# Kernel tuning notes

Hardware: AMD Instinct MI355X
Metric: run time of the kernel (lower is better)

Reference implementation:

```python
import jax, jax.numpy as jnp
import numpy as np

HIDDEN = 1024
NH = 4
DK = 1024          # key_dim = hidden * expand_k
DV = 2048          # value_dim = hidden * expand_v
HDK = DK // NH     # 256
HDV = DV // NH     # 512
LOWRANK = 16
GATE_NORM = 16.0
CHUNK = 64
EPS = 1e-5


def setup_inputs() -> dict:
    key = jax.random.key(0)
    ks = jax.random.split(key, 10)
    s = 0.02  # xavier-ish init scale (gain 2**-2.5)
    return {
        "hidden_states": jax.random.normal(ks[0], (4, 2048, HIDDEN), dtype=jnp.float32),
        "Wq": jax.random.normal(ks[1], (HIDDEN, DK), dtype=jnp.float32) * s,
        "Wk": jax.random.normal(ks[2], (HIDDEN, DK), dtype=jnp.float32) * s,
        "Wv": jax.random.normal(ks[3], (HIDDEN, DV), dtype=jnp.float32) * s,
        "Wg": jax.random.normal(ks[4], (HIDDEN, DV), dtype=jnp.float32) * s,
        "Wgk1": jax.random.normal(ks[5], (HIDDEN, LOWRANK), dtype=jnp.float32) * s,
        "Wgk2": jax.random.normal(ks[6], (LOWRANK, DK), dtype=jnp.float32) * s,
        "bgk2": jnp.zeros((DK,), dtype=jnp.float32),
        "g_norm_w": jnp.ones((HDV,), dtype=jnp.float32),
        "Wo": jax.random.normal(ks[7], (DV, HIDDEN), dtype=jnp.float32) * s,
    }


def _gla_chunked(q, k, v, gk):
    """Chunked gated linear attention.
    q, k, gk: [B, H, L, dk]; v: [B, H, L, dv]. Recurrence:
      S_t = diag(exp(gk_t)) S_{t-1} + k_t^T v_t ; o_t = (q_t * scale) S_t
    """
    B, H, L, dk = q.shape
    dv = v.shape[-1]
    N = L // CHUNK
    scale = dk ** -0.5

    def split(x):  # [B,H,L,d] -> [N,B,H,C,d]
        x = x.reshape(B, H, N, CHUNK, x.shape[-1])
        return jnp.moveaxis(x, 2, 0)

    qc, kc, vc, gc = split(q), split(k), split(v), split(gk)
    mask = jnp.tril(jnp.ones((CHUNK, CHUNK), dtype=bool))

    def step(S, inp):
        q_c, k_c, v_c, g_c = inp                 # [B,H,C,dk] / [B,H,C,dv]
        b = jnp.cumsum(g_c, axis=2)              # inclusive cumulative log-decay
        b_last = b[:, :, -1:, :]                 # [B,H,1,dk]
        q_g = q_c * jnp.exp(b) * scale           # decayed queries
        k_intra = k_c * jnp.exp(-b)              # for intra-chunk scores
        k_state = k_c * jnp.exp(b_last - b)      # for state update
        # intra-chunk causal scores: s_ij = q_i k_j exp(b_i - b_j), j <= i
        scores = jnp.einsum('bhid,bhjd->bhij', q_g, k_intra)
        scores = jnp.where(mask, scores, 0.0)
        o_intra = jnp.einsum('bhij,bhjv->bhiv', scores, v_c)
        o_inter = jnp.einsum('bhid,bhdv->bhiv', q_g, S)
        S_new = S * jnp.exp(b_last[:, :, 0, :])[..., None] \
            + jnp.einsum('bhcd,bhcv->bhdv', k_state, v_c)
        return S_new, o_intra + o_inter

    S0 = jnp.zeros((B, H, dk, dv), dtype=q.dtype)
    _, o = jax.lax.scan(step, S0, (qc, kc, vc, gc))
    o = jnp.moveaxis(o, 0, 2).reshape(B, H, L, dv)
    return o


def reference(hidden_states, Wq, Wk, Wv, Wg, Wgk1, Wgk2, bgk2, g_norm_w, Wo):
    B, L, _ = hidden_states.shape
    h = hidden_states

    def heads(x, hd):  # [B,L,H*hd] -> [B,H,L,hd]
        return x.reshape(B, L, NH, hd).transpose(0, 2, 1, 3)

    q = heads(h @ Wq, HDK)
    k = heads(h @ Wk, HDK)
    v = heads(h @ Wv, HDV)
    gk_raw = (h @ Wgk1) @ Wgk2 + bgk2
    gk = jax.nn.log_sigmoid(gk_raw) / GATE_NORM
    gk = heads(gk, HDK)

    o = _gla_chunked(q, k, v, gk)                # [B,H,L,hdv]
    o = o.transpose(0, 2, 1, 3)                  # [B,L,H,hdv]

    # FusedRMSNormSwishGate: rmsnorm(o) * silu(g), per head_v_dim
    g = (h @ Wg).reshape(B, L, NH, HDV)
    rms = o * jax.lax.rsqrt(jnp.mean(o * o, axis=-1, keepdims=True) + EPS)
    o = rms * g_norm_w * (g * jax.nn.sigmoid(g))
    o = o.reshape(B, L, DV)
    return o @ Wo
```

## Files before the change

kernel.cpp:

```cpp
#include <hip/hip_runtime.h>
#include <stdint.h>


typedef float f32x4 __attribute__((ext_vector_type(4)));
typedef short s16x8 __attribute__((ext_vector_type(8)));
typedef short s16x4 __attribute__((ext_vector_type(4)));

#define DEVINL __device__ __forceinline__

DEVINL short f2bf(float f) {
  union { float f; uint32_t u; } v; v.f = f;
  uint32_t r = v.u + 0x7fffu + ((v.u >> 16) & 1u);
  return (short)(r >> 16);
}
DEVINL float bf2f(short s) {
  union { uint32_t u; float f; } v; v.u = ((uint32_t)(uint16_t)s) << 16;
  return v.f;
}
DEVINL f32x4 mfma16(s16x8 a, s16x8 b, f32x4 c) {
  return __builtin_amdgcn_mfma_f32_16x16x32_bf16(a, b, c, 0, 0, 0);
}
#define ASYNC_COPY16(G, L)                                                   \
  __builtin_amdgcn_global_load_lds(                                          \
      (__attribute__((address_space(1))) void*)(void*)(G),                   \
      (__attribute__((address_space(3))) void*)(L), 16, 0, 0)

__global__ __launch_bounds__(256) void cvt_f2b_vec(const float* __restrict__ src,
                                                   short* __restrict__ dst) {
  int id = blockIdx.x * 256 + threadIdx.x;
  f32x4 v = ((const f32x4*)src)[id];
  s16x4 o = { f2bf(v[0]), f2bf(v[1]), f2bf(v[2]), f2bf(v[3]) };
  ((s16x4*)dst)[id] = o;
}

__global__ __launch_bounds__(256) void transpose_weights(
    const float* __restrict__ Wq, const float* __restrict__ Wk,
    const float* __restrict__ Wv, const float* __restrict__ Wg,
    const float* __restrict__ Wo, short* __restrict__ wT,
    short* __restrict__ woT) {
  __shared__ short sh[64 * 66];
  const float* src; short* dst; int K, N;
  switch (blockIdx.z) {
    case 0: src = Wq; dst = wT;                         K = 1024; N = 1024; break;
    case 1: src = Wk; dst = wT + (size_t)1024 * 1024;   K = 1024; N = 1024; break;
    case 2: src = Wv; dst = wT + (size_t)2048 * 1024;   K = 1024; N = 2048; break;
    case 3: src = Wg; dst = wT + (size_t)4096 * 1024;   K = 1024; N = 2048; break;
    default: src = Wo; dst = woT;                       K = 2048; N = 1024; break;
  }
  int n0 = blockIdx.x * 64, k0 = blockIdx.y * 64;
  if (n0 >= N || k0 >= K) return;
  int tx = threadIdx.x & 63, ty = threadIdx.x >> 6;
#pragma unroll
  for (int j = 0; j < 16; j++) {
    int r = j * 4 + ty;
    sh[r * 66 + tx] = f2bf(src[(size_t)(k0 + r) * N + n0 + tx]);
  }
  __syncthreads();
#pragma unroll
  for (int j = 0; j < 16; j++) {
    int r = j * 4 + ty;
    dst[(size_t)(n0 + r) * K + k0 + tx] = sh[tx * 66 + r];
  }
}

__global__ __launch_bounds__(256) void transpose_s16_batched(const short* __restrict__ src,
                                                             short* __restrict__ dst,
                                                             int K, int N) {
  __shared__ short sh[64 * 66];
  size_t boff = (size_t)blockIdx.z * K * N;
  int n0 = blockIdx.x * 64, k0 = blockIdx.y * 64;
  int tx = threadIdx.x & 63, ty = threadIdx.x >> 6;
#pragma unroll
  for (int j = 0; j < 16; j++) {
    int r = j * 4 + ty;
    sh[r * 66 + tx] = src[boff + (size_t)(k0 + r) * N + n0 + tx];
  }
  __syncthreads();
#pragma unroll
  for (int j = 0; j < 16; j++) {
    int r = j * 4 + ty;
    dst[boff + (size_t)(n0 + r) * K + k0 + tx] = sh[tx * 66 + r];
  }
}

__global__ __launch_bounds__(256) void gk_fused(const float* __restrict__ h,
                                                const float* __restrict__ W1,
                                                const float* __restrict__ W2,
                                                const float* __restrict__ b2,
                                                float* __restrict__ gk) {
  __shared__ float pbuf[32][8][16];
  __shared__ float hl[32][16];
  const int tid = threadIdx.x;
  const int tok0 = blockIdx.x * 32;
  {
    const int tok = tid >> 3, kg = tid & 7;
    const float* hrow = h + (size_t)(tok0 + tok) * 1024 + kg * 128;
    float p[16];
#pragma unroll
    for (int c = 0; c < 16; c++) p[c] = 0.f;
    for (int i = 0; i < 128; i++) {
      float hv = hrow[i];
      const float* wrow = W1 + (size_t)(kg * 128 + i) * 16;
#pragma unroll
      for (int c = 0; c < 16; c++) p[c] += hv * wrow[c];
    }
#pragma unroll
    for (int c = 0; c < 16; c++) pbuf[tok][kg][c] = p[c];
  }
  __syncthreads();
  for (int o = tid; o < 512; o += 256) {
    int tok = o >> 4, c = o & 15;
    float s = 0.f;
#pragma unroll
    for (int g = 0; g < 8; g++) s += pbuf[tok][g][c];
    hl[tok][c] = s;
  }
  __syncthreads();
#pragma unroll
  for (int j = 0; j < 4; j++) {
    int n = j * 256 + tid;
    float w[16];
#pragma unroll
    for (int c = 0; c < 16; c++) w[c] = W2[c * 1024 + n];
    float bias = b2[n];
    for (int t = 0; t < 32; t++) {
      float raw = bias;
#pragma unroll
      for (int c = 0; c < 16; c++) raw += hl[t][c] * w[c];
      float ls = fminf(raw, 0.f) - log1pf(__expf(-fabsf(raw)));
      gk[(size_t)(tok0 + t) * 1024 + n] = ls * 0.0625f;
    }
  }
}

template <int MODE>
__global__ __launch_bounds__(256) void gemm_bf16(const short* __restrict__ A,
                                                 const short* __restrict__ Bt, int K,
                                                 short* __restrict__ oQ,
                                                 short* __restrict__ oK,
                                                 short* __restrict__ oV,
                                                 short* __restrict__ oG,
                                                 float* __restrict__ oD) {
  __shared__ short ldsA[128 * 64];
  __shared__ short ldsB[128 * 64];
  const int tid = threadIdx.x;
  const int w = tid >> 6, lane = tid & 63;
  const int wm = w >> 1, wn = w & 1;
  const int nwg = gridDim.x * gridDim.y;
  const int orig = blockIdx.y * gridDim.x + blockIdx.x;
  const int wgid = (orig & 7) * (nwg >> 3) + (orig >> 3);
  const int bx = wgid % gridDim.x, by = wgid / gridDim.x;
  const int rowA0 = bx * 128, rowB0 = by * 128;
  f32x4 acc[4][4];
#pragma unroll
  for (int m = 0; m < 4; m++)
#pragma unroll
    for (int n = 0; n < 4; n++) acc[m][n] = (f32x4){0.f, 0.f, 0.f, 0.f};

  for (int kt = 0; kt < K; kt += 64) {
#pragma unroll
    for (int i = 0; i < 4; i++) {
      int X = i * 4096 + tid * 16;
      int r = X >> 7;
      int cB = (X & 127) ^ ((r & 7) << 4);
      ASYNC_COPY16((const char*)A + ((size_t)(rowA0 + r) * K + kt) * 2 + cB,
                   (char*)ldsA + X);
      ASYNC_COPY16((const char*)Bt + ((size_t)(rowB0 + r) * K + kt) * 2 + cB,
                   (char*)ldsB + X);
    }
    __syncthreads();
#pragma unroll
    for (int kk = 0; kk < 2; kk++) {
      s16x8 af[4], bfv[4];
#pragma unroll
      for (int mt = 0; mt < 4; mt++) {
        int row = wm * 64 + mt * 16 + (lane & 15);
        int lin = row * 128 + (kk * 32 + 8 * (lane >> 4)) * 2;
        af[mt] = *(const s16x8*)((const char*)ldsA + (lin ^ ((row & 7) << 4)));
      }
#pragma unroll
      for (int nt = 0; nt < 4; nt++) {
        int rowb = wn * 64 + nt * 16 + (lane & 15);
        int lin = rowb * 128 + (kk * 32 + 8 * (lane >> 4)) * 2;
        bfv[nt] = *(const s16x8*)((const char*)ldsB + (lin ^ ((rowb & 7) << 4)));
      }
#pragma unroll
      for (int mt = 0; mt < 4; mt++)
#pragma unroll
        for (int nt = 0; nt < 4; nt++) acc[mt][nt] = mfma16(af[mt], bfv[nt], acc[mt][nt]);
    }
    __syncthreads();
  }
#pragma unroll
  for (int mt = 0; mt < 4; mt++) {
#pragma unroll
    for (int nt = 0; nt < 4; nt++) {
      int grow0 = rowA0 + wm * 64 + mt * 16 + 4 * (lane >> 4);
      int gcol = rowB0 + wn * 64 + nt * 16 + (lane & 15);
#pragma unroll
      for (int r = 0; r < 4; r++) {
        int grow = grow0 + r;
        float val = acc[mt][nt][r];
        if (MODE == 0) {
          int sec = gcol >> 10;
          if (sec == 0)      oQ[(size_t)grow * 1024 + gcol] = f2bf(val);
          else if (sec == 1) oK[(size_t)grow * 1024 + (gcol - 1024)] = f2bf(val);
          else if (sec < 4)  oV[(size_t)grow * 2048 + (gcol - 2048)] = f2bf(val);
          else               oG[(size_t)grow * 2048 + (gcol - 4096)] = f2bf(val);
        } else {
          oD[(size_t)grow * 1024 + gcol] = val;
        }
      }
    }
  }
}

__global__ __launch_bounds__(256) void gla_intra(const short* __restrict__ Qb,
                                                 const short* __restrict__ Kb,
                                                 const float* __restrict__ gkp,
                                                 const short* __restrict__ VbT,
                                                 short* __restrict__ qg_g,
                                                 short* __restrict__ ksT_g,
                                                 float* __restrict__ Adec,
                                                 short* __restrict__ obA) {
  __shared__ short qgbuf[64 * 256];
  __shared__ short kibuf[64 * 256];
  __shared__ short scorebuf[64 * 64];
  __shared__ float adecs[256];

  const int ch = blockIdx.x, bh = blockIdx.y;
  const int b = bh >> 2, h = bh & 3;
  const int tok0 = b * 2048 + ch * 64;
  const int ltk0 = ch * 64;
  const int tid = threadIdx.x;
  const int col = h * 256 + tid;

  const float scale_ = 0.0625f;
  float cs = 0.f;
#pragma unroll 4
  for (int t = 0; t < 64; t++) {
    size_t ri = (size_t)(tok0 + t) * 1024 + col;
    cs += gkp[ri];
    float qv = bf2f(Qb[ri]);
    float kv = bf2f(Kb[ri]);
    float ep = __expf(cs);
    float en = __expf(-cs);
    short qb = f2bf(qv * ep * scale_);
    short kb = f2bf(kv * en);
    int lin = t * 512 + tid * 2;
    int sw = (t & 7) << 4;
    *(short*)((char*)qgbuf + (lin ^ sw)) = qb;
    *(short*)((char*)kibuf + (lin ^ sw)) = kb;
    qg_g[ri] = qb;
  }
  float elast = __expf(cs);
  Adec[(bh * 32 + ch) * 256 + tid] = elast;
  adecs[tid] = elast;
  __syncthreads();

  const int w = tid >> 6, lane = tid & 63;
  {
    f32x4 sc[4];
#pragma unroll
    for (int nt = 0; nt < 4; nt++) sc[nt] = (f32x4){0.f, 0.f, 0.f, 0.f};
#pragma unroll
    for (int kk = 0; kk < 8; kk++) {
      int row = 16 * w + (lane & 15);
      int lin = row * 512 + (kk * 32 + 8 * (lane >> 4)) * 2;
      s16x8 a = *(const s16x8*)((const char*)qgbuf + (lin ^ ((row & 7) << 4)));
#pragma unroll
      for (int nt = 0; nt < 4; nt++) {
        int tj = nt * 16 + (lane & 15);
        int linb = tj * 512 + (kk * 32 + 8 * (lane >> 4)) * 2;
        s16x8 bb = *(const s16x8*)((const char*)kibuf + (linb ^ ((tj & 7) << 4)));
        sc[nt] = mfma16(a, bb, sc[nt]);
      }
    }
#pragma unroll
    for (int nt = 0; nt < 4; nt++) {
#pragma unroll
      for (int r = 0; r < 4; r++) {
        int ri = 16 * w + 4 * (lane >> 4) + r;
        int cj = nt * 16 + (lane & 15);
        float v = (cj <= ri) ? sc[nt][r] : 0.f;
        int lin = ri * 128 + cj * 2;
        *(short*)((char*)scorebuf + (lin ^ ((ri & 7) << 4))) = f2bf(v);
      }
    }
  }
  __syncthreads();

  size_t ksb = (size_t)(bh * 32 + ch) * 16384;
#pragma unroll
  for (int j = 0; j < 8; j++) {
    int E = j * 2048 + tid * 8;
    int d = E >> 6, t0 = E & 63;
    float el = adecs[d];
    s16x8 v;
#pragma unroll
    for (int r = 0; r < 8; r++) {
      int t = t0 + r;
      short ki = *(const short*)((const char*)kibuf + ((t * 512 + d * 2) ^ ((t & 7) << 4)));
      v[r] = f2bf(bf2f(ki) * el);
    }
    *(s16x8*)(ksT_g + ksb + E) = v;
  }

  {
    s16x8 a2[2];
#pragma unroll
    for (int kk = 0; kk < 2; kk++) {
      int row = 16 * w + (lane & 15);
      int lin = row * 128 + (kk * 32 + 8 * (lane >> 4)) * 2;
      a2[kk] = *(const s16x8*)((const char*)scorebuf + (lin ^ ((row & 7) << 4)));
    }
    for (int nt = 0; nt < 32; nt++) {
      int e = nt * 16 + (lane & 15);
      f32x4 oacc = (f32x4){0.f, 0.f, 0.f, 0.f};
#pragma unroll
      for (int kk = 0; kk < 2; kk++) {
        const s16x8 bb = *(const s16x8*)(VbT + ((size_t)bh * 512 + e) * 2048 + ltk0 + kk * 32 + 8 * (lane >> 4));
        oacc = mfma16(a2[kk], bb, oacc);
      }
#pragma unroll
      for (int r = 0; r < 4; r++) {
        int ri = 16 * w + 4 * (lane >> 4) + r;
        obA[(size_t)(tok0 + ri) * 2048 + h * 512 + e] = f2bf(oacc[r]);
      }
    }
  }
}

__global__ __launch_bounds__(512) void gla_scan(const short* __restrict__ qg_g,
                                                const short* __restrict__ ksT_g,
                                                const short* __restrict__ VbT,
                                                const float* __restrict__ Adec,
                                                short* __restrict__ obB) {
  __shared__ short st[32 * 256];
  const int seg = blockIdx.x, bh = blockIdx.y;
  const int b = bh >> 2, h = bh & 3;
  const int tid = threadIdx.x;
  const int w = tid >> 6, lane = tid & 63;
  const int tt = w & 3;
  const int dh = w >> 2;

  f32x4 S[2][2];
#pragma unroll
  for (int mt = 0; mt < 2; mt++)
#pragma unroll
    for (int nt = 0; nt < 2; nt++) S[mt][nt] = (f32x4){0.f, 0.f, 0.f, 0.f};

  for (int ch = 0; ch < 32; ch++) {
    const int tok0 = b * 2048 + ch * 64;
    const int ltk0 = ch * 64;

#pragma unroll
    for (int mt = 0; mt < 2; mt++) {
#pragma unroll
      for (int nt = 0; nt < 2; nt++) {
        int dv = nt * 16 + (lane & 15);
        int dk0 = 32 * w + mt * 16 + 4 * (lane >> 4);
        s16x4 pk = { f2bf(S[mt][nt][0]), f2bf(S[mt][nt][1]), f2bf(S[mt][nt][2]), f2bf(S[mt][nt][3]) };
        int lin = dv * 512 + dk0 * 2;
        *(s16x4*)((char*)st + (lin ^ ((dv & 7) << 4))) = pk;
      }
    }
    __syncthreads();

    {
      s16x8 aq[8];
#pragma unroll
      for (int kk = 0; kk < 8; kk++) {
        int ti = tok0 + 16 * tt + (lane & 15);
        aq[kk] = *(const s16x8*)(qg_g + (size_t)ti * 1024 + h * 256 + kk * 32 + 8 * (lane >> 4));
      }
      f32x4 oi0 = (f32x4){0.f, 0.f, 0.f, 0.f};
      f32x4 oi1 = (f32x4){0.f, 0.f, 0.f, 0.f};
      int dv = 16 * dh + (lane & 15);
#pragma unroll
      for (int kk = 0; kk < 8; kk += 2) {
        int lin0 = dv * 512 + (kk * 32 + 8 * (lane >> 4)) * 2;
        int lin1 = dv * 512 + ((kk + 1) * 32 + 8 * (lane >> 4)) * 2;
        s16x8 b0 = *(const s16x8*)((const char*)st + (lin0 ^ ((dv & 7) << 4)));
        s16x8 b1 = *(const s16x8*)((const char*)st + (lin1 ^ ((dv & 7) << 4)));
        oi0 = mfma16(aq[kk], b0, oi0);
        oi1 = mfma16(aq[kk + 1], b1, oi1);
      }
#pragma unroll
      for (int r = 0; r < 4; r++) {
        int ti = tok0 + 16 * tt + 4 * (lane >> 4) + r;
        obB[(size_t)ti * 2048 + h * 512 + seg * 32 + 16 * dh + (lane & 15)] =
            f2bf(oi0[r] + oi1[r]);
      }
    }

#pragma unroll
    for (int mt = 0; mt < 2; mt++) {
      int dkb = 32 * w + mt * 16 + 4 * (lane >> 4);
      f32x4 a = *(const f32x4*)(Adec + (size_t)(bh * 32 + ch) * 256 + dkb);
#pragma unroll
      for (int nt = 0; nt < 2; nt++) {
        S[mt][nt][0] *= a[0]; S[mt][nt][1] *= a[1];
        S[mt][nt][2] *= a[2]; S[mt][nt][3] *= a[3];
      }
    }

    size_t ksb = (size_t)(bh * 32 + ch) * 16384;
#pragma unroll
    for (int kk = 0; kk < 2; kk++) {
      s16x8 ak[2];
#pragma unroll
      for (int mt = 0; mt < 2; mt++) {
        int dk = 32 * w + mt * 16 + (lane & 15);
        ak[mt] = *(const s16x8*)(ksT_g + ksb + (size_t)dk * 64 + kk * 32 + 8 * (lane >> 4));
      }
#pragma unroll
      for (int nt = 0; nt < 2; nt++) {
        int e = seg * 32 + nt * 16 + (lane & 15);
        s16x8 bv = *(const s16x8*)(VbT + ((size_t)bh * 512 + e) * 2048 + ltk0 + kk * 32 + 8 * (lane >> 4));
#pragma unroll
        for (int mt = 0; mt < 2; mt++) S[mt][nt] = mfma16(ak[mt], bv, S[mt][nt]);
      }
    }
    __syncthreads();
  }
}

__global__ __launch_bounds__(256) void gate_norm(const short* __restrict__ obA,
                                                 const short* __restrict__ obB,
                                                 const short* __restrict__ Gb,
                                                 const float* __restrict__ gnw,
                                                 short* __restrict__ gated) {
  int row = blockIdx.x, tid = threadIdx.x;
  int lane = tid & 63;
  size_t base = (size_t)row * 2048 + (tid >> 6) * 512 + lane * 8;
  s16x8 av = *(const s16x8*)(obA + base);
  s16x8 bv = *(const s16x8*)(obB + base);
  s16x8 gv = *(const s16x8*)(Gb + base);
  float o[8];
  float ss = 0.f;
#pragma unroll
  for (int j = 0; j < 8; j++) {
    o[j] = bf2f(av[j]) + bf2f(bv[j]);
    ss += o[j] * o[j];
  }
#pragma unroll
  for (int off = 32; off > 0; off >>= 1) ss += __shfl_xor(ss, off);
  float rinv = rsqrtf(ss * (1.0f / 512.0f) + 1e-5f);
  f32x4 w0 = *(const f32x4*)(gnw + lane * 8);
  f32x4 w1 = *(const f32x4*)(gnw + lane * 8 + 4);
  s16x8 out;
#pragma unroll
  for (int j = 0; j < 8; j++) {
    float g = bf2f(gv[j]);
    float sg = g / (1.f + __expf(-g));
    float wj = (j < 4) ? w0[j] : w1[j - 4];
    out[j] = f2bf(o[j] * rinv * wj * sg);
  }
  *(s16x8*)(gated + base) = out;
}

extern "C" void kernel_launch(void* const* d_in, const int* in_sizes, int n_in,
                              void* d_out, int out_size, void* d_ws, size_t ws_size,
                              hipStream_t stream) {
  const float* hsrc = (const float*)d_in[0];
  const float* Wq   = (const float*)d_in[1];
  const float* Wk   = (const float*)d_in[2];
  const float* Wv   = (const float*)d_in[3];
  const float* Wg   = (const float*)d_in[4];
  const float* Wgk1 = (const float*)d_in[5];
  const float* Wgk2 = (const float*)d_in[6];
  const float* bgk2 = (const float*)d_in[7];
  const float* gnw  = (const float*)d_in[8];
  const float* Wo   = (const float*)d_in[9];
  float* out = (float*)d_out;

  short* hbf = (short*)d_ws;
  short* wT  = hbf + (size_t)8192 * 1024;
  short* woT = wT + (size_t)6144 * 1024;
  short* Qb  = woT + (size_t)1024 * 2048;
  short* Kb  = Qb + (size_t)8192 * 1024;
  short* Vb  = Kb + (size_t)8192 * 1024;
  short* Gb  = Vb + (size_t)8192 * 2048;
  short* VbT = Gb + (size_t)8192 * 2048;
  short* ksT = VbT + (size_t)8192 * 2048;
  short* obA = ksT + (size_t)16 * 32 * 256 * 64;
  float* gkb = (float*)(obA + (size_t)8192 * 2048);
  float* Adec = gkb + (size_t)8192 * 1024;
  short* qg    = hbf;
  short* gated = Vb;
  short* obB   = (short*)d_out;

  cvt_f2b_vec<<<8192, 256, 0, stream>>>(hsrc, hbf);
  transpose_weights<<<dim3(32, 32, 5), 256, 0, stream>>>(Wq, Wk, Wv, Wg, Wo, wT, woT);
  gk_fused<<<256, 256, 0, stream>>>(hsrc, Wgk1, Wgk2, bgk2, gkb);
  gemm_bf16<0><<<dim3(64, 48), 256, 0, stream>>>(hbf, wT, 1024, Qb, Kb, Vb, Gb, nullptr);
  transpose_s16_batched<<<dim3(32, 32, 4), 256, 0, stream>>>(Vb, VbT, 2048, 2048);
  gla_intra<<<dim3(32, 16), 256, 0, stream>>>(Qb, Kb, gkb, VbT, qg, ksT, Adec, obA);
  gla_scan<<<dim3(16, 16), 512, 0, stream>>>(qg, ksT, VbT, Adec, obB);
  gate_norm<<<8192, 256, 0, stream>>>(obA, obB, Gb, gnw, gated);
  gemm_bf16<1><<<dim3(64, 8), 256, 0, stream>>>(gated, woT, 2048, nullptr, nullptr, nullptr, nullptr, out);
}
```

Before: 652.9 us.

## Split GLA scan into state precompute and four parallel chunk segments

Adds a gla_state kernel that runs the state recurrence and saves bf16 states at chunk boundaries 8, 16 and 24. gla_scan then launches with a z-dimension of 4, so each block seeds from a saved state and processes only 8 chunks. This is meant to give more parallelism to the serial scan on a GPU with many CUs, at the cost of an extra kernel and a bf16 rounding of the seed states. It also stages the obA writes through LDS so they are coalesced, remaps the GEMM block-to-tile order for locality, and raises wave priority around the MFMA loop.

```diff
diff --git a/kernel.cpp b/kernel.cpp
--- a/kernel.cpp
+++ b/kernel.cpp
@@ -146,10 +146,22 @@
   const int tid = threadIdx.x;
   const int w = tid >> 6, lane = tid & 63;
   const int wm = w >> 1, wn = w & 1;
-  const int nwg = gridDim.x * gridDim.y;
-  const int orig = blockIdx.y * gridDim.x + blockIdx.x;
-  const int wgid = (orig & 7) * (nwg >> 3) + (orig >> 3);
-  const int bx = wgid % gridDim.x, by = wgid / gridDim.x;
+  int bx, by;
+  {
+    const int orig = blockIdx.y * gridDim.x + blockIdx.x;
+    const int x = orig & 7;
+    const int j = orig >> 3;
+    if (MODE == 0) {
+      const int rx = x & 3, ry = x >> 2;
+      const int sub = j >> 6, t = j & 63;
+      const int sx = sub & 1, sy = sub >> 1;
+      bx = rx * 16 + sx * 8 + (t & 7);
+      by = ry * 24 + sy * 8 + (t >> 3);
+    } else {
+      bx = x * 8 + (j & 7);
+      by = j >> 3;
+    }
+  }
   const int rowA0 = bx * 128, rowB0 = by * 128;
   f32x4 acc[4][4];
 #pragma unroll
@@ -223,10 +235,11 @@
                                                  short* __restrict__ ksT_g,
                                                  float* __restrict__ Adec,
                                                  short* __restrict__ obA) {
-  __shared__ short qgbuf[64 * 256];
-  __shared__ short kibuf[64 * 256];
+  __shared__ short smem[64 * 512];
   __shared__ short scorebuf[64 * 64];
   __shared__ float adecs[256];
+  short* qgbuf = smem;
+  short* kibuf = smem + 64 * 256;
 
   const int ch = blockIdx.x, bh = blockIdx.y;
   const int b = bh >> 2, h = bh & 3;
@@ -305,6 +318,7 @@
     }
     *(s16x8*)(ksT_g + ksb + E) = v;
   }
+  __syncthreads();
 
   {
     s16x8 a2[2];
@@ -325,7 +339,89 @@
 #pragma unroll
       for (int r = 0; r < 4; r++) {
         int ri = 16 * w + 4 * (lane >> 4) + r;
-        obA[(size_t)(tok0 + ri) * 2048 + h * 512 + e] = f2bf(oacc[r]);
+        int lin3 = ri * 1024 + e * 2;
+        *(short*)((char*)smem + (lin3 ^ ((ri & 7) << 4))) = f2bf(oacc[r]);
+      }
+    }
+  }
+  __syncthreads();
+#pragma unroll
+  for (int it = 0; it < 16; it++) {
+    int row = it * 4 + (tid >> 6);
+    int vec = tid & 63;
+    int lin = row * 1024 + vec * 16;
+    s16x8 v = *(const s16x8*)((const char*)smem + (lin ^ ((row & 7) << 4)));
+    *(s16x8*)(obA + (size_t)(tok0 + row) * 2048 + h * 512 + vec * 8) = v;
+  }
+}
+
+__global__ __launch_bounds__(256) void gla_state(const short* __restrict__ ksT_g,
+                                                 const short* __restrict__ VbT,
+                                                 const float* __restrict__ Adec,
+                                                 short* __restrict__ Sb) {
+  __shared__ short st[32 * 256];
+  const int seg = blockIdx.x, bh = blockIdx.y;
+  const int tid = threadIdx.x;
+  const int w = tid >> 6, lane = tid & 63;
+
+  f32x4 S[4][2];
+#pragma unroll
+  for (int mt = 0; mt < 4; mt++)
+#pragma unroll
+    for (int nt = 0; nt < 2; nt++) S[mt][nt] = (f32x4){0.f, 0.f, 0.f, 0.f};
+
+  for (int ch = 0; ch < 24; ch++) {
+    const int ltk0 = ch * 64;
+#pragma unroll
+    for (int mt = 0; mt < 4; mt++) {
+      int dkb = 64 * w + mt * 16 + 4 * (lane >> 4);
+      f32x4 a = *(const f32x4*)(Adec + (size_t)(bh * 32 + ch) * 256 + dkb);
+#pragma unroll
+      for (int nt = 0; nt < 2; nt++) {
+        S[mt][nt][0] *= a[0]; S[mt][nt][1] *= a[1];
+        S[mt][nt][2] *= a[2]; S[mt][nt][3] *= a[3];
+      }
+    }
+    size_t ksb = (size_t)(bh * 32 + ch) * 16384;
+#pragma unroll
+    for (int kk = 0; kk < 2; kk++) {
+      s16x8 ak[4];
+#pragma unroll
+      for (int mt = 0; mt < 4; mt++) {
+        int dk = 64 * w + mt * 16 + (lane & 15);
+        ak[mt] = *(const s16x8*)(ksT_g + ksb + (size_t)dk * 64 + kk * 32 + 8 * (lane >> 4));
+      }
+#pragma unroll
+      for (int nt = 0; nt < 2; nt++) {
+        int e = seg * 32 + nt * 16 + (lane & 15);
+        s16x8 bv = *(const s16x8*)(VbT + ((size_t)bh * 512 + e) * 2048 + ltk0 + kk * 32 + 8 * (lane >> 4));
+#pragma unroll
+        for (int mt = 0; mt < 4; mt++) S[mt][nt] = mfma16(ak[mt], bv, S[mt][nt]);
+      }
+    }
+    if (ch == 7 || ch == 15 || ch == 23) {
+      int g = (ch - 7) >> 3;
+      __syncthreads();
+#pragma unroll
+      for (int mt = 0; mt < 4; mt++) {
+#pragma unroll
+        for (int nt = 0; nt < 2; nt++) {
+          int dv = nt * 16 + (lane & 15);
+          int dk0 = 64 * w + mt * 16 + 4 * (lane >> 4);
+          s16x4 pk = { f2bf(S[mt][nt][0]), f2bf(S[mt][nt][1]), f2bf(S[mt][nt][2]), f2bf(S[mt][nt][3]) };
+          int lin = dv * 512 + dk0 * 2;
+          *(s16x4*)((char*)st + (lin ^ ((dv & 7) << 4))) = pk;
+        }
+      }
+      __syncthreads();
+      char* dstb = (char*)Sb + (((size_t)(g * 16 + bh) * 512 + seg * 32) * 256) * 2;
+#pragma unroll
+      for (int it = 0; it < 4; it++) {
+        int dv = it * 8 + (tid >> 5);
+        int vec = tid & 31;
+        int X = dv * 512 + vec * 16;
+        s16x8 v = *(const s16x8*)((const char*)st + (X ^ ((dv & 7) << 4)));
+        *(s16x8*)(dstb + X) = v;
       }
     }
   }
@@ -335,14 +431,16 @@
                                                 const short* __restrict__ ksT_g,
                                                 const short* __restrict__ VbT,
                                                 const float* __restrict__ Adec,
+                                                const short* __restrict__ Sb,
                                                 short* __restrict__ obB) {
   __shared__ short st[32 * 256];
-  const int seg = blockIdx.x, bh = blockIdx.y;
+  const int seg = blockIdx.x, bh = blockIdx.y, gz = blockIdx.z;
   const int b = bh >> 2, h = bh & 3;
   const int tid = threadIdx.x;
   const int w = tid >> 6, lane = tid & 63;
   const int tt = w & 3;
   const int dh = w >> 2;
+  const int ch0 = gz * 8;
 
   f32x4 S[2][2];
 #pragma unroll
@@ -350,19 +448,46 @@
 #pragma unroll
     for (int nt = 0; nt < 2; nt++) S[mt][nt] = (f32x4){0.f, 0.f, 0.f, 0.f};
 
-  for (int ch = 0; ch < 32; ch++) {
-    const int tok0 = b * 2048 + ch * 64;
-    const int ltk0 = ch * 64;
-
+  if (gz > 0) {
+    const char* srcb = (const char*)Sb + ((((size_t)(gz - 1) * 16 + bh) * 512 + seg * 32) * 256) * 2;
+#pragma unroll
+    for (int it = 0; it < 2; it++) {
+      int dv = it * 16 + (tid >> 5);
+      int vec = tid & 31;
+      int X = dv * 512 + vec * 16;
+      s16x8 v = *(const s16x8*)(srcb + X);
+      *(s16x8*)((char*)st + (X ^ ((dv & 7) << 4))) = v;
+    }
+    __syncthreads();
 #pragma unroll
     for (int mt = 0; mt < 2; mt++) {
 #pragma unroll
       for (int nt = 0; nt < 2; nt++) {
         int dv = nt * 16 + (lane & 15);
         int dk0 = 32 * w + mt * 16 + 4 * (lane >> 4);
-        s16x4 pk = { f2bf(S[mt][nt][0]), f2bf(S[mt][nt][1]), f2bf(S[mt][nt][2]), f2bf(S[mt][nt][3]) };
         int lin = dv * 512 + dk0 * 2;
-        *(s16x4*)((char*)st + (lin ^ ((dv & 7) << 4))) = pk;
+        s16x4 pk = *(const s16x4*)((const char*)st + (lin ^ ((dv & 7) << 4)));
+        S[mt][nt][0] = bf2f(pk[0]); S[mt][nt][1] = bf2f(pk[1]);
+        S[mt][nt][2] = bf2f(pk[2]); S[mt][nt][3] = bf2f(pk[3]);
+      }
+    }
+  }
+
+  for (int ch = ch0; ch < ch0 + 8; ch++) {
+    const int tok0 = b * 2048 + ch * 64;
+    const int ltk0 = ch * 64;
+
+    if (ch != ch0 || gz == 0) {
+#pragma unroll
+      for (int mt = 0; mt < 2; mt++) {
+#pragma unroll
+        for (int nt = 0; nt < 2; nt++) {
+          int dv = nt * 16 + (lane & 15);
+          int dk0 = 32 * w + mt * 16 + 4 * (lane >> 4);
+          s16x4 pk = { f2bf(S[mt][nt][0]), f2bf(S[mt][nt][1]), f2bf(S[mt][nt][2]), f2bf(S[mt][nt][3]) };
+          int lin = dv * 512 + dk0 * 2;
+          *(s16x4*)((char*)st + (lin ^ ((dv & 7) << 4))) = pk;
+        }
       }
     }
     __syncthreads();
@@ -377,6 +502,7 @@
       f32x4 oi0 = (f32x4){0.f, 0.f, 0.f, 0.f};
       f32x4 oi1 = (f32x4){0.f, 0.f, 0.f, 0.f};
       int dv = 16 * dh + (lane & 15);
+      __builtin_amdgcn_s_setprio(1);
 #pragma unroll
       for (int kk = 0; kk < 8; kk += 2) {
         int lin0 = dv * 512 + (kk * 32 + 8 * (lane >> 4)) * 2;
@@ -386,6 +512,7 @@
         oi0 = mfma16(aq[kk], b0, oi0);
         oi1 = mfma16(aq[kk + 1], b1, oi1);
       }
+      __builtin_amdgcn_s_setprio(0);
 #pragma unroll
       for (int r = 0; r < 4; r++) {
         int ti = tok0 + 16 * tt + 4 * (lane >> 4) + r;
@@ -487,6 +614,7 @@
   short* obA = ksT + (size_t)16 * 32 * 256 * 64;
   float* gkb = (float*)(obA + (size_t)8192 * 2048);
   float* Adec = gkb + (size_t)8192 * 1024;
+  short* Sb  = (short*)(Adec + (size_t)16 * 32 * 256);
   short* qg    = hbf;
   short* gated = Vb;
   short* obB   = (short*)d_out;
@@ -497,7 +625,8 @@
   gemm_bf16<0><<<dim3(64, 48), 256, 0, stream>>>(hbf, wT, 1024, Qb, Kb, Vb, Gb, nullptr);
   transpose_s16_batched<<<dim3(32, 32, 4), 256, 0, stream>>>(Vb, VbT, 2048, 2048);
   gla_intra<<<dim3(32, 16), 256, 0, stream>>>(Qb, Kb, gkb, VbT, qg, ksT, Adec, obA);
-  gla_scan<<<dim3(16, 16), 512, 0, stream>>>(qg, ksT, VbT, Adec, obB);
+  gla_state<<<dim3(16, 16), 256, 0, stream>>>(ksT, VbT, Adec, Sb);
+  gla_scan<<<dim3(16, 16, 4), 512, 0, stream>>>(qg, ksT, VbT, Adec, Sb, obB);
   gate_norm<<<8192, 256, 0, stream>>>(obA, obB, Gb, gnw, gated);
   gemm_bf16<1><<<dim3(64, 8), 256, 0, stream>>>(gated, woT, 2048, nullptr, nullptr, nullptr, nullptr, out);
 }
```

New measurement: 656.6 us. Within noise of the previous version (+0.6%).
